# Performance work log

Hardware: AMD Instinct MI355X
Metric: run time of the kernel (lower is better)

The kernel has to match this reference:

```python
import jax, jax.numpy as jnp
import numpy as np

N_NODES = 50000
EPS = 1e-12  # F.normalize eps


def sage_conv(x, src, dst, W_l, b_l, W_r):
    # PyG SAGEConv: out = lin_l(mean_j x_j) + lin_r(x_i), then L2 normalize.
    n = x.shape[0]
    agg = jax.ops.segment_sum(x[src], dst, num_segments=n)          # [N, d]
    cnt = jax.ops.segment_sum(jnp.ones_like(src, dtype=x.dtype), dst,
                              num_segments=n)                       # [N]
    mean = agg / jnp.maximum(cnt, 1.0)[:, None]
    out = mean @ W_l.T + b_l + x @ W_r.T
    norm = jnp.linalg.norm(out, axis=-1, keepdims=True)
    return out / jnp.maximum(norm, EPS)


def setup_inputs() -> dict:
    key = jax.random.key(0)
    ks = jax.random.split(key, 8)
    nfeat, nhid, nclass = 64, 64, 10
    E = 1250000
    features = jax.random.normal(ks[0], (N_NODES, nfeat), dtype=jnp.float32)
    edge_index = jax.random.randint(ks[1], (2, E), 0, N_NODES, dtype=jnp.int64)
    s1 = 1.0 / np.sqrt(nfeat)
    s2 = 1.0 / np.sqrt(nhid)
    return {
        "features": features,
        "edge_index": edge_index,
        "W1_l": jax.random.normal(ks[2], (nhid, nfeat), dtype=jnp.float32) * s1,
        "b1": jnp.zeros((nhid,), dtype=jnp.float32),
        "W1_r": jax.random.normal(ks[3], (nhid, nfeat), dtype=jnp.float32) * s1,
        "W2_l": jax.random.normal(ks[4], (nclass, nhid), dtype=jnp.float32) * s2,
        "b2": jnp.zeros((nclass,), dtype=jnp.float32),
        "W2_r": jax.random.normal(ks[5], (nclass, nhid), dtype=jnp.float32) * s2,
    }


def reference(features, edge_index, W1_l, b1, W1_r, W2_l, b2, W2_r):
    src, dst = edge_index[0], edge_index[1]
    x = jax.nn.relu(sage_conv(features, src, dst, W1_l, b1, W1_r))
    # dropout is identity in eval mode
    x = sage_conv(x, src, dst, W2_l, b2, W2_r)
    return jax.nn.log_softmax(x, axis=1)
```

## Files before the change

### kernel.cpp

```cpp
#include <hip/hip_runtime.h>
#include <hip/hip_bf16.h>


static constexpr int FEAT = 64;
static constexpr int SLOTS = 64;
static constexpr int BUCK_SZ = 6250;

__device__ __forceinline__ unsigned short f2bf(float f) {
  __hip_bfloat16 h = __float2bfloat16(f);
  return *reinterpret_cast<unsigned short*>(&h);
}
__device__ __forceinline__ unsigned int pk2(float a, float b) {
  return (unsigned)f2bf(a) | ((unsigned)f2bf(b) << 16);
}
__device__ __forceinline__ float bfl(unsigned int u) {
  return __uint_as_float(u << 16);
}
__device__ __forceinline__ float bfh(unsigned int u) {
  return __uint_as_float(u & 0xFFFF0000u);
}
__device__ __forceinline__ void acc8(float* a, const uint4& w) {
  a[0] += bfl(w.x); a[1] += bfh(w.x); a[2] += bfl(w.y); a[3] += bfh(w.y);
  a[4] += bfl(w.z); a[5] += bfh(w.z); a[6] += bfl(w.w); a[7] += bfh(w.w);
}

__global__ __launch_bounds__(256) void dense1_kernel(
    const float* __restrict__ x,
    const float* __restrict__ Wl, const float* __restrict__ Wr,
    const float* __restrict__ b,
    unsigned short* __restrict__ p, float* __restrict__ q,
    int* __restrict__ cursor, uint4* __restrict__ p2z, int N) {
  __shared__ float4 Ws[64 * 16];
  int mat = blockIdx.y;
  const float4* Wg = (const float4*)(mat ? Wr : Wl);
  int tid = threadIdx.x;
#pragma unroll
  for (int i = 0; i < 4; ++i) Ws[i * 256 + tid] = Wg[i * 256 + tid];

  int node = blockIdx.x * 256 + tid;
  if (mat == 0 && node < N) cursor[node] = 0;
  __syncthreads();
  if (node >= N) {
    if (node == N && mat == 0) {
      uint4 z = make_uint4(0u, 0u, 0u, 0u);
      uint4* z1 = (uint4*)(p + (size_t)N * 64);
#pragma unroll
      for (int r = 0; r < 8; ++r) z1[r] = z;
      p2z[(size_t)N * 2] = z;
      p2z[(size_t)N * 2 + 1] = z;
    }
    return;
  }

  const float4* X4 = (const float4*)x + (size_t)node * 16;
  float4 xr[16];
#pragma unroll
  for (int kq = 0; kq < 16; ++kq) xr[kq] = X4[kq];

#pragma unroll 1
  for (int og = 0; og < 4; ++og) {
    float acc[16];
#pragma unroll 4
    for (int o = 0; o < 16; ++o) {
      float a = 0.0f;
#pragma unroll
      for (int kq = 0; kq < 16; ++kq) {
        float4 w = Ws[(og * 16 + o) * 16 + kq];
        float4 xv = xr[kq];
        a = fmaf(xv.x, w.x, fmaf(xv.y, w.y, fmaf(xv.z, w.z, fmaf(xv.w, w.w, a))));
      }
      acc[o] = a;
    }

    if (mat) {
      float4* O4 = (float4*)(q + (size_t)node * FEAT + og * 16);
      const float4* B4 = (const float4*)(b + og * 16);
#pragma unroll
      for (int oq = 0; oq < 4; ++oq) {
        float4 bv = B4[oq];
        O4[oq] = make_float4(acc[oq * 4] + bv.x, acc[oq * 4 + 1] + bv.y,
                             acc[oq * 4 + 2] + bv.z, acc[oq * 4 + 3] + bv.w);
      }
    } else {
      uint4 w0, w1;
      w0.x = pk2(acc[0], acc[1]);
      w0.y = pk2(acc[2], acc[3]);
      w0.z = pk2(acc[4], acc[5]);
      w0.w = pk2(acc[6], acc[7]);
      w1.x = pk2(acc[8], acc[9]);
      w1.y = pk2(acc[10], acc[11]);
      w1.z = pk2(acc[12], acc[13]);
      w1.w = pk2(acc[14], acc[15]);
      uint4* O = (uint4*)p + (size_t)node * 8 + og * 2;
      O[0] = w0;
      O[1] = w1;
    }
  }
}

__global__ __launch_bounds__(256) void fill_kernel(
    const int* __restrict__ src, const int* __restrict__ dst,
    int* __restrict__ cursor, unsigned short* __restrict__ col,
    int e0, int e1) {
  int b = blockIdx.x & 7;
  int e = e0 + (blockIdx.x >> 3) * 256 + threadIdx.x;
  if (e >= e1) return;
  int d = __builtin_nontemporal_load(dst + e);
  int lo = b * BUCK_SZ;
  if (d >= lo && d < lo + BUCK_SZ) {
    int s = __builtin_nontemporal_load(src + e);
    int pos = atomicAdd(&cursor[d], 1);
    if (pos < SLOTS) col[d * SLOTS + pos] = (unsigned short)s;
  }
}

__global__ __launch_bounds__(256) void gather1_dense2_kernel(
    const int* __restrict__ cursor, const unsigned short* __restrict__ col,
    const uint4* __restrict__ p1, const float* __restrict__ q1,
    const float* __restrict__ W2l, const float* __restrict__ W2r,
    const float* __restrict__ b2,
    uint4* __restrict__ p2, float* __restrict__ q2, int N) {
  __shared__ float4 Wall[2 * 10 * 17];
  __shared__ float bs[10];
  int tid = threadIdx.x;
  if (tid < 160) {
    int c = tid >> 4, k = tid & 15;
    Wall[c * 17 + k] = ((const float4*)W2l)[tid];
    Wall[170 + c * 17 + k] = ((const float4*)W2r)[tid];
  }
  if (tid < 10) bs[tid] = b2[tid];
  __syncthreads();

  int wave = tid >> 6, lane = tid & 63;
  int g = lane >> 3, q = lane & 7;
  int node = blockIdx.x * 4 + wave;
  if (node >= N) return;

  int deg = cursor[node];
  int cnt = min(deg, SLOTS);
  int beg = node * SLOTS;
  int cv = (int)col[beg + lane];

  const float4* Q4 = (const float4*)q1 + (size_t)node * 16 + q * 2;
  float4 q0 = Q4[0], q1v = Q4[1];

  float a[8];
#pragma unroll
  for (int j = 0; j < 8; ++j) a[j] = 0.0f;

  {
    int t0 = __shfl(cv, g), t1 = __shfl(cv, 8 + g);
    int t2 = __shfl(cv, 16 + g), t3 = __shfl(cv, 24 + g);
    int s0 = (g < cnt) ? t0 : N;
    int s1 = (8 + g < cnt) ? t1 : N;
    int s2 = (16 + g < cnt) ? t2 : N;
    int s3 = (24 + g < cnt) ? t3 : N;
    uint4 w0 = p1[(size_t)s0 * 8 + q];
    uint4 w1 = p1[(size_t)s1 * 8 + q];
    uint4 w2 = p1[(size_t)s2 * 8 + q];
    uint4 w3 = p1[(size_t)s3 * 8 + q];
    acc8(a, w0); acc8(a, w1); acc8(a, w2); acc8(a, w3);
  }
  if (cnt > 32) {
    int t0 = __shfl(cv, 32 + g), t1 = __shfl(cv, 40 + g);
    int t2 = __shfl(cv, 48 + g), t3 = __shfl(cv, 56 + g);
    int s0 = (32 + g < cnt) ? t0 : N;
    int s1 = (40 + g < cnt) ? t1 : N;
    int s2 = (48 + g < cnt) ? t2 : N;
    int s3 = (56 + g < cnt) ? t3 : N;
    uint4 w0 = p1[(size_t)s0 * 8 + q];
    uint4 w1 = p1[(size_t)s1 * 8 + q];
    uint4 w2 = p1[(size_t)s2 * 8 + q];
    uint4 w3 = p1[(size_t)s3 * 8 + q];
    acc8(a, w0); acc8(a, w1); acc8(a, w2); acc8(a, w3);
  }

#pragma unroll
  for (int off = 8; off <= 32; off <<= 1) {
#pragma unroll
    for (int j = 0; j < 8; ++j) a[j] += __shfl_xor(a[j], off);
  }

  float invc = 1.0f / (float)max(deg, 1);
  float v[8];
  v[0] = fmaf(a[0], invc, q0.x); v[1] = fmaf(a[1], invc, q0.y);
  v[2] = fmaf(a[2], invc, q0.z); v[3] = fmaf(a[3], invc, q0.w);
  v[4] = fmaf(a[4], invc, q1v.x); v[5] = fmaf(a[5], invc, q1v.y);
  v[6] = fmaf(a[6], invc, q1v.z); v[7] = fmaf(a[7], invc, q1v.w);

  float ss = 0.0f;
#pragma unroll
  for (int j = 0; j < 8; ++j) ss += v[j] * v[j];
#pragma unroll
  for (int off = 1; off <= 4; off <<= 1) ss += __shfl_xor(ss, off);
  float scale = 1.0f / fmaxf(sqrtf(ss), 1e-12f);

  float h[8];
#pragma unroll
  for (int j = 0; j < 8; ++j) h[j] = fmaxf(v[j] * scale, 0.0f);

  float res[3];
#pragma unroll
  for (int r = 0; r < 3; ++r) {
    int t = r * 8 + g;
    int base = (t < 10) ? 0 : 170;
    int c = (t < 10) ? t : (t - 10);
    c = min(c, 9);
    float4 wa = Wall[base + c * 17 + q * 2];
    float4 wb = Wall[base + c * 17 + q * 2 + 1];
    float pr = fmaf(h[0], wa.x, fmaf(h[1], wa.y, fmaf(h[2], wa.z,
               fmaf(h[3], wa.w, fmaf(h[4], wb.x, fmaf(h[5], wb.y,
               fmaf(h[6], wb.z, h[7] * wb.w)))))));
    pr += __shfl_xor(pr, 1);
    pr += __shfl_xor(pr, 2);
    pr += __shfl_xor(pr, 4);
    res[r] = pr;
  }

  float pv[10], qv[10];
#pragma unroll
  for (int i = 0; i < 10; ++i) {
    pv[i] = __shfl(res[i >> 3], (i & 7) * 8);
    int t2 = 10 + i;
    qv[i] = __shfl(res[t2 >> 3], (t2 & 7) * 8);
  }

  if (lane == 0) {
    uint4 w0, w1;
    w0.x = pk2(pv[0], pv[1]); w0.y = pk2(pv[2], pv[3]);
    w0.z = pk2(pv[4], pv[5]); w0.w = pk2(pv[6], pv[7]);
    w1.x = pk2(pv[8], pv[9]); w1.y = 0u; w1.z = 0u; w1.w = 0u;
    p2[(size_t)node * 2] = w0;
    p2[(size_t)node * 2 + 1] = w1;
  } else if (lane == 1) {
    *(float4*)(q2 + (size_t)node * 16) =
        make_float4(qv[0] + bs[0], qv[1] + bs[1], qv[2] + bs[2], qv[3] + bs[3]);
  } else if (lane == 2) {
    *(float4*)(q2 + (size_t)node * 16 + 4) =
        make_float4(qv[4] + bs[4], qv[5] + bs[5], qv[6] + bs[6], qv[7] + bs[7]);
  } else if (lane == 3) {
    *(float4*)(q2 + (size_t)node * 16 + 8) =
        make_float4(qv[8] + bs[8], qv[9] + bs[9], 0.f, 0.f);
  } else if (lane == 4) {
    *(float4*)(q2 + (size_t)node * 16 + 12) = make_float4(0.f, 0.f, 0.f, 0.f);
  }
}

__global__ __launch_bounds__(256) void gather2_kernel(
    const int* __restrict__ cursor, const unsigned short* __restrict__ col,
    const uint4* __restrict__ p2, const float* __restrict__ q2,
    float* __restrict__ out, int N) {
  int tid = threadIdx.x;
  int wave = tid >> 6, lane = tid & 63;
  int g = lane >> 1, q = lane & 1;
  int node = blockIdx.x * 4 + wave;
  if (node >= N) return;

  int deg = cursor[node];
  int cnt = min(deg, SLOTS);
  int beg = node * SLOTS;
  int cv = (int)col[beg + lane];

  const float4* Q4 = (const float4*)q2 + (size_t)node * 4 + q * 2;
  float4 q0 = Q4[0], q1 = Q4[1];

  float a[8];
#pragma unroll
  for (int j = 0; j < 8; ++j) a[j] = 0.0f;

  {
    int t0 = __shfl(cv, g);
    int s0 = (g < cnt) ? t0 : N;
    uint4 w0 = p2[(size_t)s0 * 2 + q];
    acc8(a, w0);
  }
  if (cnt > 32) {
    int t1 = __shfl(cv, 32 + g);
    int s1 = (32 + g < cnt) ? t1 : N;
    uint4 w1 = p2[(size_t)s1 * 2 + q];
    acc8(a, w1);
  }

#pragma unroll
  for (int off = 2; off <= 32; off <<= 1) {
#pragma unroll
    for (int j = 0; j < 8; ++j) a[j] += __shfl_xor(a[j], off);
  }

  float invc = 1.0f / (float)max(deg, 1);
  float v[8];
  v[0] = fmaf(a[0], invc, q0.x); v[1] = fmaf(a[1], invc, q0.y);
  v[2] = fmaf(a[2], invc, q0.z); v[3] = fmaf(a[3], invc, q0.w);
  v[4] = fmaf(a[4], invc, q1.x); v[5] = fmaf(a[5], invc, q1.y);
  v[6] = fmaf(a[6], invc, q1.z); v[7] = fmaf(a[7], invc, q1.w);

  float ss = 0.0f;
#pragma unroll
  for (int j = 0; j < 8; ++j) ss += v[j] * v[j];
  ss += __shfl_xor(ss, 1);
  float scale = 1.0f / fmaxf(sqrtf(ss), 1e-12f);
#pragma unroll
  for (int j = 0; j < 8; ++j) v[j] *= scale;

  float m;
  if (q == 0) {
    m = v[0];
#pragma unroll
    for (int j = 1; j < 8; ++j) m = fmaxf(m, v[j]);
  } else {
    m = fmaxf(v[0], v[1]);
  }
  m = fmaxf(m, __shfl_xor(m, 1));

  float es = 0.0f;
  if (q == 0) {
#pragma unroll
    for (int j = 0; j < 8; ++j) es += __expf(v[j] - m);
  } else {
    es = __expf(v[0] - m) + __expf(v[1] - m);
  }
  es += __shfl_xor(es, 1);
  float lse = m + __logf(es);

  if (g == 0) {
    float2* o = (float2*)(out + (size_t)node * 10);
    if (q == 0) {
      o[0] = make_float2(v[0] - lse, v[1] - lse);
      o[1] = make_float2(v[2] - lse, v[3] - lse);
      o[2] = make_float2(v[4] - lse, v[5] - lse);
      o[3] = make_float2(v[6] - lse, v[7] - lse);
    } else {
      o[4] = make_float2(v[0] - lse, v[1] - lse);
    }
  }
}

extern "C" void kernel_launch(void* const* d_in, const int* in_sizes, int n_in,
                              void* d_out, int out_size, void* d_ws, size_t ws_size,
                              hipStream_t stream) {
  const float* features = (const float*)d_in[0];
  const int* edge_index = (const int*)d_in[1];
  const float* W1_l = (const float*)d_in[2];
  const float* b1   = (const float*)d_in[3];
  const float* W1_r = (const float*)d_in[4];
  const float* W2_l = (const float*)d_in[5];
  const float* b2   = (const float*)d_in[6];
  const float* W2_r = (const float*)d_in[7];
  float* out = (float*)d_out;

  const int N = in_sizes[0] / FEAT;
  const int E = in_sizes[1] / 2;
  const int* src = edge_index;
  const int* dst = edge_index + E;

  char* ws = (char*)d_ws;
  int* cursor            = (int*)(ws + 0);
  unsigned short* col    = (unsigned short*)(ws + 200064);
  unsigned short* p1     = (unsigned short*)(ws + 6600064);
  float* q1              = (float*)(ws + 13000192);
  uint4* p2              = (uint4*)(ws + 25800192);
  float* q2              = (float*)(ws + 27400256);

  int Eh = E / 2;
  int ebh = ((Eh + 255) / 256) * 8;
  int nb256 = (N + 255) / 256;
  int nbw = (N + 3) / 4;

  dense1_kernel<<<dim3(nb256, 2), 256, 0, stream>>>(
      features, W1_l, W1_r, b1, p1, q1, cursor, p2, N);
  fill_kernel<<<ebh, 256, 0, stream>>>(src, dst, cursor, col, 0, Eh);
  fill_kernel<<<ebh, 256, 0, stream>>>(src, dst, cursor, col, Eh, E);
  gather1_dense2_kernel<<<nbw, 256, 0, stream>>>(
      cursor, col, (const uint4*)p1, q1, W2_l, W2_r, b2, p2, q2, N);
  gather2_kernel<<<nbw, 256, 0, stream>>>(
      cursor, col, (const uint4*)p2, q2, out, N);
}
```

Before: 235.3 us.

## Split dense1 over output groups, use packed f32 math and 32-bit gather offsets

dense1 now launches one block per (matrix, 16-output group), so each block stages only a quarter of the weights in shared memory and there are four times as many blocks. The gather kernels switch to packed v_pk_add/fma/mul f32 inline asm for accumulation, normalisation and the small matvec. Neighbour addresses become 32-bit byte offsets instead of 64-bit index math. The trade-off is that each row of x is reloaded four times in dense1, and inline asm can block compiler scheduling.

```diff
diff --git a/kernel.cpp b/kernel.cpp
--- a/kernel.cpp
+++ b/kernel.cpp
@@ -6,6 +6,8 @@
 static constexpr int SLOTS = 64;
 static constexpr int BUCK_SZ = 6250;
 
+typedef float v2f __attribute__((ext_vector_type(2)));
+
 __device__ __forceinline__ unsigned short f2bf(float f) {
   __hip_bfloat16 h = __float2bfloat16(f);
   return *reinterpret_cast<unsigned short*>(&h);
@@ -13,15 +15,30 @@
 __device__ __forceinline__ unsigned int pk2(float a, float b) {
   return (unsigned)f2bf(a) | ((unsigned)f2bf(b) << 16);
 }
-__device__ __forceinline__ float bfl(unsigned int u) {
-  return __uint_as_float(u << 16);
-}
-__device__ __forceinline__ float bfh(unsigned int u) {
-  return __uint_as_float(u & 0xFFFF0000u);
-}
-__device__ __forceinline__ void acc8(float* a, const uint4& w) {
-  a[0] += bfl(w.x); a[1] += bfh(w.x); a[2] += bfl(w.y); a[3] += bfh(w.y);
-  a[4] += bfl(w.z); a[5] += bfh(w.z); a[6] += bfl(w.w); a[7] += bfh(w.w);
+__device__ __forceinline__ void pkacc(v2f& acc, v2f v) {
+  asm("v_pk_add_f32 %0, %1, %0" : "+v"(acc) : "v"(v));
+}
+__device__ __forceinline__ v2f pkfma(v2f a, v2f b, v2f c) {
+  v2f d;
+  asm("v_pk_fma_f32 %0, %1, %2, %3" : "=v"(d) : "v"(a), "v"(b), "v"(c));
+  return d;
+}
+__device__ __forceinline__ v2f pkmul(v2f a, v2f b) {
+  v2f d;
+  asm("v_pk_mul_f32 %0, %1, %2" : "=v"(d) : "v"(a), "v"(b));
+  return d;
+}
+__device__ __forceinline__ void accu2(v2f& acc, unsigned u) {
+  v2f t;
+  t.x = __uint_as_float(u << 16);
+  t.y = __uint_as_float(u & 0xFFFF0000u);
+  pkacc(acc, t);
+}
+__device__ __forceinline__ void acc8p(v2f* a, const uint4& w) {
+  accu2(a[0], w.x); accu2(a[1], w.y); accu2(a[2], w.z); accu2(a[3], w.w);
+}
+__device__ __forceinline__ uint4 ld16(const void* base, unsigned byteoff) {
+  return *(const uint4*)((const char*)base + byteoff);
 }
 
 __global__ __launch_bounds__(256) void dense1_kernel(
@@ -30,18 +47,18 @@
     const float* __restrict__ b,
     unsigned short* __restrict__ p, float* __restrict__ q,
     int* __restrict__ cursor, uint4* __restrict__ p2z, int N) {
-  __shared__ float4 Ws[64 * 16];
-  int mat = blockIdx.y;
+  __shared__ float4 Ws[16 * 16];
+  int mat = blockIdx.y >> 2;
+  int og = blockIdx.y & 3;
   const float4* Wg = (const float4*)(mat ? Wr : Wl);
   int tid = threadIdx.x;
-#pragma unroll
-  for (int i = 0; i < 4; ++i) Ws[i * 256 + tid] = Wg[i * 256 + tid];
+  Ws[tid] = Wg[(og * 16) * 16 + tid];
 
   int node = blockIdx.x * 256 + tid;
-  if (mat == 0 && node < N) cursor[node] = 0;
+  if (blockIdx.y == 0 && node < N) cursor[node] = 0;
   __syncthreads();
   if (node >= N) {
-    if (node == N && mat == 0) {
+    if (node == N && blockIdx.y == 0) {
       uint4 z = make_uint4(0u, 0u, 0u, 0u);
       uint4* z1 = (uint4*)(p + (size_t)N * 64);
 #pragma unroll
@@ -57,44 +74,41 @@
 #pragma unroll
   for (int kq = 0; kq < 16; ++kq) xr[kq] = X4[kq];
 
-#pragma unroll 1
-  for (int og = 0; og < 4; ++og) {
-    float acc[16];
+  float acc[16];
 #pragma unroll 4
-    for (int o = 0; o < 16; ++o) {
-      float a = 0.0f;
-#pragma unroll
-      for (int kq = 0; kq < 16; ++kq) {
-        float4 w = Ws[(og * 16 + o) * 16 + kq];
-        float4 xv = xr[kq];
-        a = fmaf(xv.x, w.x, fmaf(xv.y, w.y, fmaf(xv.z, w.z, fmaf(xv.w, w.w, a))));
-      }
-      acc[o] = a;
-    }
-
-    if (mat) {
-      float4* O4 = (float4*)(q + (size_t)node * FEAT + og * 16);
-      const float4* B4 = (const float4*)(b + og * 16);
-#pragma unroll
-      for (int oq = 0; oq < 4; ++oq) {
-        float4 bv = B4[oq];
-        O4[oq] = make_float4(acc[oq * 4] + bv.x, acc[oq * 4 + 1] + bv.y,
-                             acc[oq * 4 + 2] + bv.z, acc[oq * 4 + 3] + bv.w);
-      }
-    } else {
-      uint4 w0, w1;
-      w0.x = pk2(acc[0], acc[1]);
-      w0.y = pk2(acc[2], acc[3]);
-      w0.z = pk2(acc[4], acc[5]);
-      w0.w = pk2(acc[6], acc[7]);
-      w1.x = pk2(acc[8], acc[9]);
-      w1.y = pk2(acc[10], acc[11]);
-      w1.z = pk2(acc[12], acc[13]);
-      w1.w = pk2(acc[14], acc[15]);
-      uint4* O = (uint4*)p + (size_t)node * 8 + og * 2;
-      O[0] = w0;
-      O[1] = w1;
-    }
+  for (int o = 0; o < 16; ++o) {
+    float a = 0.0f;
+#pragma unroll
+    for (int kq = 0; kq < 16; ++kq) {
+      float4 w = Ws[o * 16 + kq];
+      float4 xv = xr[kq];
+      a = fmaf(xv.x, w.x, fmaf(xv.y, w.y, fmaf(xv.z, w.z, fmaf(xv.w, w.w, a))));
+    }
+    acc[o] = a;
+  }
+
+  if (mat) {
+    float4* O4 = (float4*)(q + (size_t)node * FEAT + og * 16);
+    const float4* B4 = (const float4*)(b + og * 16);
+#pragma unroll
+    for (int oq = 0; oq < 4; ++oq) {
+      float4 bv = B4[oq];
+      O4[oq] = make_float4(acc[oq * 4] + bv.x, acc[oq * 4 + 1] + bv.y,
+                           acc[oq * 4 + 2] + bv.z, acc[oq * 4 + 3] + bv.w);
+    }
+  } else {
+    uint4 w0, w1;
+    w0.x = pk2(acc[0], acc[1]);
+    w0.y = pk2(acc[2], acc[3]);
+    w0.z = pk2(acc[4], acc[5]);
+    w0.w = pk2(acc[6], acc[7]);
+    w1.x = pk2(acc[8], acc[9]);
+    w1.y = pk2(acc[10], acc[11]);
+    w1.z = pk2(acc[12], acc[13]);
+    w1.w = pk2(acc[14], acc[15]);
+    uint4* O = (uint4*)p + (size_t)node * 8 + og * 2;
+    O[0] = w0;
+    O[1] = w1;
   }
 }
 
@@ -116,7 +130,7 @@
 
 __global__ __launch_bounds__(256) void gather1_dense2_kernel(
     const int* __restrict__ cursor, const unsigned short* __restrict__ col,
-    const uint4* __restrict__ p1, const float* __restrict__ q1,
+    const void* __restrict__ p1, const float* __restrict__ q1,
     const float* __restrict__ W2l, const float* __restrict__ W2r,
     const float* __restrict__ b2,
     uint4* __restrict__ p2, float* __restrict__ q2, int N) {
@@ -140,64 +154,81 @@
   int cnt = min(deg, SLOTS);
   int beg = node * SLOTS;
   int cv = (int)col[beg + lane];
+  unsigned qoff = (unsigned)q << 4;
 
   const float4* Q4 = (const float4*)q1 + (size_t)node * 16 + q * 2;
   float4 q0 = Q4[0], q1v = Q4[1];
 
-  float a[8];
-#pragma unroll
-  for (int j = 0; j < 8; ++j) a[j] = 0.0f;
+  v2f a2[4];
+#pragma unroll
+  for (int k = 0; k < 4; ++k) { a2[k].x = 0.0f; a2[k].y = 0.0f; }
 
   {
     int t0 = __shfl(cv, g), t1 = __shfl(cv, 8 + g);
     int t2 = __shfl(cv, 16 + g), t3 = __shfl(cv, 24 + g);
-    int s0 = (g < cnt) ? t0 : N;
-    int s1 = (8 + g < cnt) ? t1 : N;
-    int s2 = (16 + g < cnt) ? t2 : N;
-    int s3 = (24 + g < cnt) ? t3 : N;
-    uint4 w0 = p1[(size_t)s0 * 8 + q];
-    uint4 w1 = p1[(size_t)s1 * 8 + q];
-    uint4 w2 = p1[(size_t)s2 * 8 + q];
-    uint4 w3 = p1[(size_t)s3 * 8 + q];
-    acc8(a, w0); acc8(a, w1); acc8(a, w2); acc8(a, w3);
+    unsigned o0 = ((unsigned)((g < cnt) ? t0 : N) << 7) + qoff;
+    unsigned o1 = ((unsigned)((8 + g < cnt) ? t1 : N) << 7) + qoff;
+    unsigned o2 = ((unsigned)((16 + g < cnt) ? t2 : N) << 7) + qoff;
+    unsigned o3 = ((unsigned)((24 + g < cnt) ? t3 : N) << 7) + qoff;
+    uint4 w0 = ld16(p1, o0);
+    uint4 w1 = ld16(p1, o1);
+    uint4 w2 = ld16(p1, o2);
+    uint4 w3 = ld16(p1, o3);
+    acc8p(a2, w0); acc8p(a2, w1); acc8p(a2, w2); acc8p(a2, w3);
   }
   if (cnt > 32) {
     int t0 = __shfl(cv, 32 + g), t1 = __shfl(cv, 40 + g);
     int t2 = __shfl(cv, 48 + g), t3 = __shfl(cv, 56 + g);
-    int s0 = (32 + g < cnt) ? t0 : N;
-    int s1 = (40 + g < cnt) ? t1 : N;
-    int s2 = (48 + g < cnt) ? t2 : N;
-    int s3 = (56 + g < cnt) ? t3 : N;
-    uint4 w0 = p1[(size_t)s0 * 8 + q];
-    uint4 w1 = p1[(size_t)s1 * 8 + q];
-    uint4 w2 = p1[(size_t)s2 * 8 + q];
-    uint4 w3 = p1[(size_t)s3 * 8 + q];
-    acc8(a, w0); acc8(a, w1); acc8(a, w2); acc8(a, w3);
+    unsigned o0 = ((unsigned)((32 + g < cnt) ? t0 : N) << 7) + qoff;
+    unsigned o1 = ((unsigned)((40 + g < cnt) ? t1 : N) << 7) + qoff;
+    unsigned o2 = ((unsigned)((48 + g < cnt) ? t2 : N) << 7) + qoff;
+    unsigned o3 = ((unsigned)((56 + g < cnt) ? t3 : N) << 7) + qoff;
+    uint4 w0 = ld16(p1, o0);
+    uint4 w1 = ld16(p1, o1);
+    uint4 w2 = ld16(p1, o2);
+    uint4 w3 = ld16(p1, o3);
+    acc8p(a2, w0); acc8p(a2, w1); acc8p(a2, w2); acc8p(a2, w3);
   }
 
 #pragma unroll
   for (int off = 8; off <= 32; off <<= 1) {
 #pragma unroll
-    for (int j = 0; j < 8; ++j) a[j] += __shfl_xor(a[j], off);
+    for (int k = 0; k < 4; ++k) {
+      v2f t;
+      t.x = __shfl_xor(a2[k].x, off);
+      t.y = __shfl_xor(a2[k].y, off);
+      pkacc(a2[k], t);
+    }
   }
 
   float invc = 1.0f / (float)max(deg, 1);
-  float v[8];
-  v[0] = fmaf(a[0], invc, q0.x); v[1] = fmaf(a[1], invc, q0.y);
-  v[2] = fmaf(a[2], invc, q0.z); v[3] = fmaf(a[3], invc, q0.w);
-  v[4] = fmaf(a[4], invc, q1v.x); v[5] = fmaf(a[5], invc, q1v.y);
-  v[6] = fmaf(a[6], invc, q1v.z); v[7] = fmaf(a[7], invc, q1v.w);
-
-  float ss = 0.0f;
-#pragma unroll
-  for (int j = 0; j < 8; ++j) ss += v[j] * v[j];
+  v2f invc2; invc2.x = invc; invc2.y = invc;
+  v2f c0; c0.x = q0.x; c0.y = q0.y;
+  v2f c1; c1.x = q0.z; c1.y = q0.w;
+  v2f c2; c2.x = q1v.x; c2.y = q1v.y;
+  v2f c3; c3.x = q1v.z; c3.y = q1v.w;
+  v2f v0 = pkfma(a2[0], invc2, c0);
+  v2f v1 = pkfma(a2[1], invc2, c1);
+  v2f v2_ = pkfma(a2[2], invc2, c2);
+  v2f v3 = pkfma(a2[3], invc2, c3);
+
+  v2f ssp = pkmul(v0, v0);
+  ssp = pkfma(v1, v1, ssp);
+  ssp = pkfma(v2_, v2_, ssp);
+  ssp = pkfma(v3, v3, ssp);
+  float ss = ssp.x + ssp.y;
 #pragma unroll
   for (int off = 1; off <= 4; off <<= 1) ss += __shfl_xor(ss, off);
   float scale = 1.0f / fmaxf(sqrtf(ss), 1e-12f);
 
+  v2f s2; s2.x = scale; s2.y = scale;
+  v2f g0 = pkmul(v0, s2), g1 = pkmul(v1, s2);
+  v2f g2 = pkmul(v2_, s2), g3 = pkmul(v3, s2);
   float h[8];
-#pragma unroll
-  for (int j = 0; j < 8; ++j) h[j] = fmaxf(v[j] * scale, 0.0f);
+  h[0] = fmaxf(g0.x, 0.f); h[1] = fmaxf(g0.y, 0.f);
+  h[2] = fmaxf(g1.x, 0.f); h[3] = fmaxf(g1.y, 0.f);
+  h[4] = fmaxf(g2.x, 0.f); h[5] = fmaxf(g2.y, 0.f);
+  h[6] = fmaxf(g3.x, 0.f); h[7] = fmaxf(g3.y, 0.f);
 
   float res[3];
 #pragma unroll
@@ -208,9 +239,19 @@
     c = min(c, 9);
     float4 wa = Wall[base + c * 17 + q * 2];
     float4 wb = Wall[base + c * 17 + q * 2 + 1];
-    float pr = fmaf(h[0], wa.x, fmaf(h[1], wa.y, fmaf(h[2], wa.z,
-               fmaf(h[3], wa.w, fmaf(h[4], wb.x, fmaf(h[5], wb.y,
-               fmaf(h[6], wb.z, h[7] * wb.w)))))));
+    v2f ha; ha.x = h[0]; ha.y = h[1];
+    v2f hb; hb.x = h[2]; hb.y = h[3];
+    v2f hc; hc.x = h[4]; hc.y = h[5];
+    v2f hd; hd.x = h[6]; hd.y = h[7];
+    v2f wa0; wa0.x = wa.x; wa0.y = wa.y;
+    v2f wa1; wa1.x = wa.z; wa1.y = wa.w;
+    v2f wb0; wb0.x = wb.x; wb0.y = wb.y;
+    v2f wb1; wb1.x = wb.z; wb1.y = wb.w;
+    v2f pp = pkmul(ha, wa0);
+    pp = pkfma(hb, wa1, pp);
+    pp = pkfma(hc, wb0, pp);
+    pp = pkfma(hd, wb1, pp);
+    float pr = pp.x + pp.y;
     pr += __shfl_xor(pr, 1);
     pr += __shfl_xor(pr, 2);
     pr += __shfl_xor(pr, 4);
@@ -248,7 +289,7 @@
 
 __global__ __launch_bounds__(256) void gather2_kernel(
     const int* __restrict__ cursor, const unsigned short* __restrict__ col,
-    const uint4* __restrict__ p2, const float* __restrict__ q2,
+    const void* __restrict__ p2, const float* __restrict__ q2,
     float* __restrict__ out, int N) {
   int tid = threadIdx.x;
   int wave = tid >> 6, lane = tid & 63;
@@ -260,47 +301,64 @@
   int cnt = min(deg, SLOTS);
   int beg = node * SLOTS;
   int cv = (int)col[beg + lane];
+  unsigned qoff = (unsigned)q << 4;
 
   const float4* Q4 = (const float4*)q2 + (size_t)node * 4 + q * 2;
   float4 q0 = Q4[0], q1 = Q4[1];
 
-  float a[8];
-#pragma unroll
-  for (int j = 0; j < 8; ++j) a[j] = 0.0f;
+  v2f a2[4];
+#pragma unroll
+  for (int k = 0; k < 4; ++k) { a2[k].x = 0.0f; a2[k].y = 0.0f; }
 
   {
     int t0 = __shfl(cv, g);
-    int s0 = (g < cnt) ? t0 : N;
-    uint4 w0 = p2[(size_t)s0 * 2 + q];
-    acc8(a, w0);
+    unsigned o0 = ((unsigned)((g < cnt) ? t0 : N) << 5) + qoff;
+    uint4 w0 = ld16(p2, o0);
+    acc8p(a2, w0);
   }
   if (cnt > 32) {
     int t1 = __shfl(cv, 32 + g);
-    int s1 = (32 + g < cnt) ? t1 : N;
-    uint4 w1 = p2[(size_t)s1 * 2 + q];
-    acc8(a, w1);
+    unsigned o1 = ((unsigned)((32 + g < cnt) ? t1 : N) << 5) + qoff;
+    uint4 w1 = ld16(p2, o1);
+    acc8p(a2, w1);
   }
 
 #pragma unroll
   for (int off = 2; off <= 32; off <<= 1) {
 #pragma unroll
-    for (int j = 0; j < 8; ++j) a[j] += __shfl_xor(a[j], off);
+    for (int k = 0; k < 4; ++k) {
+      v2f t;
+      t.x = __shfl_xor(a2[k].x, off);
+      t.y = __shfl_xor(a2[k].y, off);
+      pkacc(a2[k], t);
+    }
   }
 
   float invc = 1.0f / (float)max(deg, 1);
-  float v[8];
-  v[0] = fmaf(a[0], invc, q0.x); v[1] = fmaf(a[1], invc, q0.y);
-  v[2] = fmaf(a[2], invc, q0.z); v[3] = fmaf(a[3], invc, q0.w);
-  v[4] = fmaf(a[4], invc, q1.x); v[5] = fmaf(a[5], invc, q1.y);
-  v[6] = fmaf(a[6], invc, q1.z); v[7] = fmaf(a[7], invc, q1.w);
-
-  float ss = 0.0f;
-#pragma unroll
-  for (int j = 0; j < 8; ++j) ss += v[j] * v[j];
+  v2f invc2; invc2.x = invc; invc2.y = invc;
+  v2f c0; c0.x = q0.x; c0.y = q0.y;
+  v2f c1; c1.x = q0.z; c1.y = q0.w;
+  v2f c2; c2.x = q1.x; c2.y = q1.y;
+  v2f c3; c3.x = q1.z; c3.y = q1.w;
+  v2f u0 = pkfma(a2[0], invc2, c0);
+  v2f u1 = pkfma(a2[1], invc2, c1);
+  v2f u2 = pkfma(a2[2], invc2, c2);
+  v2f u3 = pkfma(a2[3], invc2, c3);
+
+  v2f ssp = pkmul(u0, u0);
+  ssp = pkfma(u1, u1, ssp);
+  ssp = pkfma(u2, u2, ssp);
+  ssp = pkfma(u3, u3, ssp);
+  float ss = ssp.x + ssp.y;
   ss += __shfl_xor(ss, 1);
   float scale = 1.0f / fmaxf(sqrtf(ss), 1e-12f);
-#pragma unroll
-  for (int j = 0; j < 8; ++j) v[j] *= scale;
+
+  v2f s2; s2.x = scale; s2.y = scale;
+  u0 = pkmul(u0, s2); u1 = pkmul(u1, s2);
+  u2 = pkmul(u2, s2); u3 = pkmul(u3, s2);
+  float v[8];
+  v[0] = u0.x; v[1] = u0.y; v[2] = u1.x; v[3] = u1.y;
+  v[4] = u2.x; v[5] = u2.y; v[6] = u3.x; v[7] = u3.y;
 
   float m;
   if (q == 0) {
@@ -366,12 +424,12 @@
   int nb256 = (N + 255) / 256;
   int nbw = (N + 3) / 4;
 
-  dense1_kernel<<<dim3(nb256, 2), 256, 0, stream>>>(
+  dense1_kernel<<<dim3(nb256, 8), 256, 0, stream>>>(
       features, W1_l, W1_r, b1, p1, q1, cursor, p2, N);
   fill_kernel<<<ebh, 256, 0, stream>>>(src, dst, cursor, col, 0, Eh);
   fill_kernel<<<ebh, 256, 0, stream>>>(src, dst, cursor, col, Eh, E);
   gather1_dense2_kernel<<<nbw, 256, 0, stream>>>(
-      cursor, col, (const uint4*)p1, q1, W2_l, W2_r, b2, p2, q2, N);
+      cursor, col, (const void*)p1, q1, W2_l, W2_r, b2, p2, q2, N);
   gather2_kernel<<<nbw, 256, 0, stream>>>(
-      cursor, col, (const uint4*)p2, q2, out, N);
-}
+      cursor, col, (const void*)p2, q2, out, N);
+}
```

Result: faster. 230.4 us (-2.1%).
